# Performance work log

Measured on AMD Instinct MI355X. Metric: run time of the kernel, lower is better.

## Reference

```python
import jax, jax.numpy as jnp
import numpy as np


def setup_inputs() -> dict:
    key = jax.random.key(0)
    kq, kk, kv = jax.random.split(key, 3)
    B, H, S, D = 2, 16, 2048, 64
    Q = jax.random.normal(kq, (B, H, S, D), dtype=jnp.float32)
    K = jax.random.normal(kk, (B, H, S, D), dtype=jnp.float32)
    V = jax.random.normal(kv, (B, H, S, D), dtype=jnp.float32)
    # causal mask: 1 = keep, 0 = masked (masked_fill on mask == 0)
    mask = jnp.tril(jnp.ones((S, S), dtype=bool))[None, None, :, :]
    return {"V": V, "Q": Q, "K": K, "Fk": D, "mask": mask}


def reference(V, Q, K, Fk, mask):
    scale = 1.0 / jnp.sqrt(jnp.asarray(Fk, dtype=jnp.float32))
    # [B,H,S,S] scores
    C = jnp.einsum("bhqd,bhkd->bhqk", Q, K) * scale
    C = jnp.where(mask, C, jnp.asarray(-1e9, dtype=C.dtype))
    C = jax.nn.softmax(C, axis=-1)
    return jnp.einsum("bhqk,bhkd->bhqd", C, V)
```

## Files before the change

### kernel.cpp

```cpp
#include <hip/hip_runtime.h>
#include <hip/hip_bf16.h>

typedef __bf16 bf16x8 __attribute__((ext_vector_type(8)));
typedef __bf16 bf16x4 __attribute__((ext_vector_type(4)));
typedef __bf16 bf16x2 __attribute__((ext_vector_type(2)));
typedef float f32x4 __attribute__((ext_vector_type(4)));
typedef float f32x16 __attribute__((ext_vector_type(16)));

#define S_LEN 2048
#define D_DIM 64
#define NQT   32

static __device__ __forceinline__ unsigned pk2(float a, float b) {
  bf16x2 t; t[0] = (__bf16)a; t[1] = (__bf16)b;
  return __builtin_bit_cast(unsigned, t);
}

__global__ __launch_bounds__(256) void preprocess_kernel(
    const float* __restrict__ Kg, const float* __restrict__ Vg,
    unsigned char* __restrict__ Kb, unsigned char* __restrict__ Vt) {
  __shared__ float buf[2048];
  const int tid  = threadIdx.x;
  const int tile = blockIdx.x;
  const float* kg = Kg + (long)tile * 2048;
  const float* vg = Vg + (long)tile * 2048;
  unsigned char* kb = Kb + (long)tile * 4096;
  unsigned char* vt = Vt + (long)tile * 4096;

  const int l = tid & 63, f = tid >> 6, h = l >> 5;

  {
    const float* kr = kg + (l & 31) * 64 + f * 16 + h * 8;
    float4 a = *reinterpret_cast<const float4*>(kr);
    float4 b = *reinterpret_cast<const float4*>(kr + 4);
    bf16x8 t;
    t[0]=(__bf16)a.x; t[1]=(__bf16)a.y; t[2]=(__bf16)a.z; t[3]=(__bf16)a.w;
    t[4]=(__bf16)b.x; t[5]=(__bf16)b.y; t[6]=(__bf16)b.z; t[7]=(__bf16)b.w;
    *reinterpret_cast<bf16x8*>(kb + tid * 16) = t;
  }
  #pragma unroll
  for (int i = 0; i < 2; ++i) {
    int idx = tid + 256 * i;
    *reinterpret_cast<float4*>(buf + idx * 4) =
        *reinterpret_cast<const float4*>(vg + idx * 4);
  }
  __syncthreads();
  {
    int dt = f >> 1, ks = f & 1;
    int d  = dt * 32 + (l & 31);
    int k0 = ks * 16 + h * 8;
    bf16x8 t;
    #pragma unroll
    for (int j = 0; j < 8; ++j) t[j] = (__bf16)buf[(k0 + j) * 64 + d];
    *reinterpret_cast<bf16x8*>(vt + tid * 16) = t;
  }
}

__global__ __launch_bounds__(256, 2) void attn_fwd_q64(
    const float* __restrict__ Qg, const unsigned char* __restrict__ Kb,
    const unsigned char* __restrict__ Vt, float* __restrict__ Og) {
  __shared__ float o_sm[4][32][68];
  __shared__ float m_sm[4][32];
  __shared__ float l_sm[4][32];

  const int tid  = threadIdx.x;
  const int lane = tid & 63;
  const int w    = tid >> 6;
  const int qc   = lane & 31;
  const int h    = lane >> 5;

  const int b  = blockIdx.x;
  const int e  = b & 7;
  const int s  = b >> 3;
  const int bh = e + 8 * (s >> 4);
  const int pi = s & 15;
  const long base = (long)bh * (S_LEN * D_DIM);

  const unsigned char* kb_bh = Kb + (long)bh * 64 * 4096 + lane * 16;
  const unsigned char* vt_bh = Vt + (long)bh * 64 * 4096 + lane * 16;

  bf16x8 kfr[4], vfr[4];
  auto ldK = [&](int kt) {
    const unsigned char* p = kb_bh + (long)kt * 4096;
    #pragma unroll
    for (int t = 0; t < 4; ++t)
      kfr[t] = *reinterpret_cast<const bf16x8*>(p + t * 1024);
  };
  auto ldV = [&](int kt) {
    const unsigned char* p = vt_bh + (long)kt * 4096;
    #pragma unroll
    for (int t = 0; t < 4; ++t)
      vfr[t] = *reinterpret_cast<const bf16x8*>(p + t * 1024);
  };

  auto process = [&](f32x16& sa, float& m_run, float& l_run,
                     f32x16& po0, f32x16& po1) {
    float rmax;
    {
      float a0 = fmaxf(fmaxf(sa[0], sa[1]),  fmaxf(sa[2], sa[3]));
      float a1 = fmaxf(fmaxf(sa[4], sa[5]),  fmaxf(sa[6], sa[7]));
      float a2 = fmaxf(fmaxf(sa[8], sa[9]),  fmaxf(sa[10], sa[11]));
      float a3 = fmaxf(fmaxf(sa[12], sa[13]), fmaxf(sa[14], sa[15]));
      rmax = fmaxf(fmaxf(a0, a1), fmaxf(a2, a3));
      rmax = fmaxf(rmax, __shfl_xor(rmax, 32));
    }
    if (__any(rmax > m_run + 8.0f)) {
      float mn    = fmaxf(m_run, rmax);
      float alpha = exp2f(m_run - mn);
      m_run = mn;
      l_run *= alpha;
      #pragma unroll
      for (int r = 0; r < 16; ++r) {
        float ar = __shfl(alpha, (r & 3) + 8 * (r >> 2) + 4 * h);
        po0[r] *= ar;
        po1[r] *= ar;
      }
    }
    #pragma unroll
    for (int r = 0; r < 16; ++r) sa[r] = exp2f(sa[r] - m_run);
    {
      float s0 = (sa[0] + sa[1]) + (sa[2] + sa[3]);
      float s1 = (sa[4] + sa[5]) + (sa[6] + sa[7]);
      float s2 = (sa[8] + sa[9]) + (sa[10] + sa[11]);
      float s3 = (sa[12] + sa[13]) + (sa[14] + sa[15]);
      float rs = (s0 + s1) + (s2 + s3);
      l_run += rs + __shfl_xor(rs, 32);
    }
    bf16x8 pa0, pa1;
    {
      unsigned k0 = pk2(sa[0], sa[1]),   k1 = pk2(sa[2], sa[3]);
      unsigned k2 = pk2(sa[4], sa[5]),   k3 = pk2(sa[6], sa[7]);
      unsigned k4 = pk2(sa[8], sa[9]),   k5 = pk2(sa[10], sa[11]);
      unsigned k6 = pk2(sa[12], sa[13]), k7 = pk2(sa[14], sa[15]);
      unsigned x02 = h ? k0 : k2, x13 = h ? k1 : k3;
      unsigned x46 = h ? k4 : k6, x57 = h ? k5 : k7;
      unsigned p02 = (unsigned)__shfl_xor((int)x02, 32);
      unsigned p13 = (unsigned)__shfl_xor((int)x13, 32);
      unsigned p46 = (unsigned)__shfl_xor((int)x46, 32);
      unsigned p57 = (unsigned)__shfl_xor((int)x57, 32);
      union { unsigned u[4]; bf16x8 v; } a2, b2;
      a2.u[0] = h ? p02 : k0;  a2.u[1] = h ? p13 : k1;
      a2.u[2] = h ? k2 : p02;  a2.u[3] = h ? k3 : p13;
      b2.u[0] = h ? p46 : k4;  b2.u[1] = h ? p57 : k5;
      b2.u[2] = h ? k6 : p46;  b2.u[3] = h ? k7 : p57;
      pa0 = a2.v;
      pa1 = b2.v;
    }
    __builtin_amdgcn_s_setprio(1);
    po0 = __builtin_amdgcn_mfma_f32_32x32x16_bf16(pa0, vfr[0], po0, 0, 0, 0);
    po0 = __builtin_amdgcn_mfma_f32_32x32x16_bf16(pa1, vfr[1], po0, 0, 0, 0);
    po1 = __builtin_amdgcn_mfma_f32_32x32x16_bf16(pa0, vfr[2], po1, 0, 0, 0);
    po1 = __builtin_amdgcn_mfma_f32_32x32x16_bf16(pa1, vfr[3], po1, 0, 0, 0);
    __builtin_amdgcn_s_setprio(0);
  };

  auto submerge = [&](const f32x16& po0, const f32x16& po1,
                      float m_run, float l_run, int qbase) {
    #pragma unroll
    for (int r = 0; r < 16; ++r) {
      int crow = (r & 3) + 8 * (r >> 2) + 4 * h;
      o_sm[w][crow][qc]      = po0[r];
      o_sm[w][crow][qc + 32] = po1[r];
    }
    if (h == 0) { m_sm[w][qc] = m_run; l_sm[w][qc] = l_run; }
    __syncthreads();
    {
      const int q  = tid >> 3;
      const int d0 = (tid & 7) * 8;
      float m0 = m_sm[0][q], m1 = m_sm[1][q];
      float m2 = m_sm[2][q], m3 = m_sm[3][q];
      float M  = fmaxf(fmaxf(m0, m1), fmaxf(m2, m3));
      float a0 = exp2f(m0 - M), a1 = exp2f(m1 - M);
      float a2 = exp2f(m2 - M), a3 = exp2f(m3 - M);
      float inv = 1.0f / (a0 * l_sm[0][q] + a1 * l_sm[1][q]
                        + a2 * l_sm[2][q] + a3 * l_sm[3][q]);
      float* og = Og + base + (long)(qbase + q) * D_DIM + d0;
      #pragma unroll
      for (int half = 0; half < 2; ++half) {
        float4 x0 = *reinterpret_cast<const float4*>(&o_sm[0][q][d0 + 4 * half]);
        float4 x1 = *reinterpret_cast<const float4*>(&o_sm[1][q][d0 + 4 * half]);
        float4 x2 = *reinterpret_cast<const float4*>(&o_sm[2][q][d0 + 4 * half]);
        float4 x3 = *reinterpret_cast<const float4*>(&o_sm[3][q][d0 + 4 * half]);
        float4 o;
        o.x = (a0 * x0.x + a1 * x1.x + a2 * x2.x + a3 * x3.x) * inv;
        o.y = (a0 * x0.y + a1 * x1.y + a2 * x2.y + a3 * x3.y) * inv;
        o.z = (a0 * x0.z + a1 * x1.z + a2 * x2.z + a3 * x3.z) * inv;
        o.w = (a0 * x0.w + a1 * x1.w + a2 * x2.w + a3 * x3.w) * inv;
        *reinterpret_cast<float4*>(og + 4 * half) = o;
      }
    }
  };

  for (int phase = 0; phase < 2; ++phase) {
    const int g  = phase ? pi : (31 - pi);
    const int q0 = g * 64;
    const int NT = 2 * g + 2;

    bf16x8 qfA[4], qfB[4];
    {
      const float qsc = 0.125f * 1.44269504f;
      const float* qpA = Qg + base + (long)(q0 + qc) * D_DIM + h * 8;
      const float* qpB = qpA + 32 * D_DIM;
      #pragma unroll
      for (int t = 0; t < 4; ++t) {
        float4 f0 = *reinterpret_cast<const float4*>(qpA + t * 16);
        float4 f1 = *reinterpret_cast<const float4*>(qpA + t * 16 + 4);
        bf16x8 q;
        q[0]=(__bf16)(f0.x*qsc); q[1]=(__bf16)(f0.y*qsc);
        q[2]=(__bf16)(f0.z*qsc); q[3]=(__bf16)(f0.w*qsc);
        q[4]=(__bf16)(f1.x*qsc); q[5]=(__bf16)(f1.y*qsc);
        q[6]=(__bf16)(f1.z*qsc); q[7]=(__bf16)(f1.w*qsc);
        qfA[t] = q;
        f0 = *reinterpret_cast<const float4*>(qpB + t * 16);
        f1 = *reinterpret_cast<const float4*>(qpB + t * 16 + 4);
        q[0]=(__bf16)(f0.x*qsc); q[1]=(__bf16)(f0.y*qsc);
        q[2]=(__bf16)(f0.z*qsc); q[3]=(__bf16)(f0.w*qsc);
        q[4]=(__bf16)(f1.x*qsc); q[5]=(__bf16)(f1.y*qsc);
        q[6]=(__bf16)(f1.z*qsc); q[7]=(__bf16)(f1.w*qsc);
        qfB[t] = q;
      }
    }

    f32x16 poA0, poA1, poB0, poB1;
    #pragma unroll
    for (int r = 0; r < 16; ++r) { poA0[r]=0.f; poA1[r]=0.f; poB0[r]=0.f; poB1[r]=0.f; }
    float mA = -1e30f, lA = 0.f, mB = -1e30f, lB = 0.f;

    ldK(w);
    ldV(w);

    for (int kt = w; kt < NT; kt += 4) {
      const bool more = (kt + 4 < NT);
      const bool doA  = (kt != NT - 1);

      f32x16 saA, saB;
      __builtin_amdgcn_s_setprio(1);
      if (doA) {
        #pragma unroll
        for (int r = 0; r < 16; ++r) saA[r] = 0.f;
        #pragma unroll
        for (int t = 0; t < 4; ++t)
          saA = __builtin_amdgcn_mfma_f32_32x32x16_bf16(kfr[t], qfA[t], saA, 0, 0, 0);
      }
      #pragma unroll
      for (int r = 0; r < 16; ++r) saB[r] = 0.f;
      #pragma unroll
      for (int t = 0; t < 4; ++t)
        saB = __builtin_amdgcn_mfma_f32_32x32x16_bf16(kfr[t], qfB[t], saB, 0, 0, 0);
      __builtin_amdgcn_s_setprio(0);

      if (more) ldK(kt + 4);

      if (kt == NT - 2) {
        #pragma unroll
        for (int r = 0; r < 16; ++r)
          if (((r & 3) + 8 * (r >> 2) + 4 * h) > qc) saA[r] = -1e30f;
      }
      if (kt == NT - 1) {
        #pragma unroll
        for (int r = 0; r < 16; ++r)
          if (((r & 3) + 8 * (r >> 2) + 4 * h) > qc) saB[r] = -1e30f;
      }

      if (doA) process(saA, mA, lA, poA0, poA1);
      process(saB, mB, lB, poB0, poB1);

      if (more) ldV(kt + 4);
    }

    if (phase) __syncthreads();
    submerge(poA0, poA1, mA, lA, q0);
    __syncthreads();
    submerge(poB0, poB1, mB, lB, q0 + 32);
  }
}

__global__ __launch_bounds__(256) void attn_fwd_fallback(
    const float* __restrict__ Vg, const float* __restrict__ Qg,
    const float* __restrict__ Kg, float* __restrict__ Og) {
  __shared__ __align__(16) unsigned char k_lds[64 * 128];
  __shared__ __align__(16) unsigned char vt_lds[64 * 128];
  __shared__ __align__(16) unsigned char p_lds[4][16 * 128];

  const int tid  = threadIdx.x;
  const int lane = tid & 63;
  const int w    = tid >> 6;
  const int lr   = lane & 15;
  const int lg   = lane >> 4;
  const int swz  = (lr & 7) << 4;

  const int lb = blockIdx.x;
  const int e  = lb & 7;
  const int s  = lb >> 3;
  const int bh = e + 8 * (s >> 5);
  const int qs = s & 31;
  const int qt = (qs & 1) ? (NQT - 1 - (qs >> 1)) : (qs >> 1);
  const long base = (long)bh * (S_LEN * D_DIM);
  const int q0 = qt * 64;

  bf16x8 qf[2];
  {
    const float qsc = 0.125f * 1.44269504f;
    const float* qp = Qg + base + (q0 + w * 16 + lr) * D_DIM + lg * 8;
    #pragma unroll
    for (int c = 0; c < 2; ++c) {
      float4 f0 = *reinterpret_cast<const float4*>(qp + c * 32);
      float4 f1 = *reinterpret_cast<const float4*>(qp + c * 32 + 4);
      bf16x8 t;
      t[0]=(__bf16)(f0.x*qsc); t[1]=(__bf16)(f0.y*qsc);
      t[2]=(__bf16)(f0.z*qsc); t[3]=(__bf16)(f0.w*qsc);
      t[4]=(__bf16)(f1.x*qsc); t[5]=(__bf16)(f1.y*qsc);
      t[6]=(__bf16)(f1.z*qsc); t[7]=(__bf16)(f1.w*qsc);
      qf[c] = t;
    }
  }
  bf16x8 onesf;
  #pragma unroll
  for (int j = 0; j < 8; ++j) onesf[j] = (lr == 0) ? (__bf16)1.0f : (__bf16)0.0f;

  f32x4 po[4], pl;
  float m_run = -1e30f;
  #pragma unroll
  for (int j = 0; j < 4; ++j) po[j] = (f32x4){0.f,0.f,0.f,0.f};
  pl = (f32x4){0.f,0.f,0.f,0.f};

  float4 kreg[4];
  float  vreg[16];
  const int d_ = lane;
  const int kb = w;

  auto load_regs = [&](int kt) {
    const float* kg = Kg + base + kt * (64 * D_DIM);
    #pragma unroll
    for (int i = 0; i < 4; ++i) {
      int idx = tid + 256 * i;
      int r = idx >> 4, f4 = idx & 15;
      kreg[i] = *reinterpret_cast<const float4*>(kg + r * 64 + f4 * 4);
    }
    const float* vg = Vg + base + kt * (64 * D_DIM);
    #pragma unroll
    for (int j = 0; j < 8; ++j) {
      vreg[j]     = vg[(kb * 8 + j) * 64 + d_];
      vreg[8 + j] = vg[((kb + 4) * 8 + j) * 64 + d_];
    }
  };
  auto write_buf = [&]() {
    #pragma unroll
    for (int i = 0; i < 4; ++i) {
      int idx = tid + 256 * i;
      int r = idx >> 4, f4 = idx & 15;
      bf16x4 t;
      t[0]=(__bf16)kreg[i].x; t[1]=(__bf16)kreg[i].y;
      t[2]=(__bf16)kreg[i].z; t[3]=(__bf16)kreg[i].w;
      int b = r * 128 + ((f4 * 8) ^ ((r & 7) << 4));
      *reinterpret_cast<bf16x4*>(&k_lds[b]) = t;
    }
    bf16x8 t0, t1;
    #pragma unroll
    for (int j = 0; j < 8; ++j) { t0[j] = (__bf16)vreg[j]; t1[j] = (__bf16)vreg[8+j]; }
    int b0 = d_ * 128 + ((kb * 16) ^ ((d_ & 7) << 4));
    int b1 = d_ * 128 + (((kb + 4) * 16) ^ ((d_ & 7) << 4));
    *reinterpret_cast<bf16x8*>(&vt_lds[b0]) = t0;
    *reinterpret_cast<bf16x8*>(&vt_lds[b1]) = t1;
  };

  load_regs(0);
  write_buf();
  __syncthreads();

  for (int kt = 0; kt <= qt; ++kt) {
    const bool last = (kt == qt);
    if (!last) load_regs(kt + 1);

    f32x4 sa[4];
    #pragma unroll
    for (int ct = 0; ct < 4; ++ct) sa[ct] = (f32x4){0.f,0.f,0.f,0.f};
    #pragma unroll
    for (int ct = 0; ct < 4; ++ct) {
      #pragma unroll
      for (int c = 0; c < 2; ++c) {
        int b = (ct * 16 + lr) * 128 + ((lg * 16 + c * 64) ^ swz);
        bf16x8 kf = *reinterpret_cast<const bf16x8*>(&k_lds[b]);
        sa[ct] = __builtin_amdgcn_mfma_f32_16x16x32_bf16(kf, qf[c], sa[ct], 0, 0, 0);
      }
    }
    if (last) {
      #pragma unroll
      for (int ct = 0; ct < 4; ++ct)
        #pragma unroll
        for (int j = 0; j < 4; ++j)
          if (ct * 16 + lg * 4 + j > w * 16 + lr) sa[ct][j] = -1e30f;
    }
    float rmax = sa[0][0];
    #pragma unroll
    for (int ct = 0; ct < 4; ++ct)
      #pragma unroll
      for (int j = 0; j < 4; ++j) rmax = fmaxf(rmax, sa[ct][j]);
    rmax = fmaxf(rmax, __shfl_xor(rmax, 16));
    rmax = fmaxf(rmax, __shfl_xor(rmax, 32));
    float mn    = fmaxf(m_run, rmax);
    float alpha = exp2f(m_run - mn);
    m_run = mn;
    #pragma unroll
    for (int ct = 0; ct < 4; ++ct) {
      bf16x4 t;
      #pragma unroll
      for (int j = 0; j < 4; ++j) t[j] = (__bf16)exp2f(sa[ct][j] - mn);
      int b = lr * 128 + ((ct * 32 + lg * 8) ^ swz);
      *reinterpret_cast<bf16x4*>(&p_lds[w][b]) = t;
    }
    float aj[4];
    #pragma unroll
    for (int j = 0; j < 4; ++j) aj[j] = __shfl(alpha, (lane & 48) | (lg * 4 + j));
    #pragma unroll
    for (int j = 0; j < 4; ++j) {
      pl[j] *= aj[j];
      #pragma unroll
      for (int dt = 0; dt < 4; ++dt) po[dt][j] *= aj[j];
    }
    #pragma unroll
    for (int c = 0; c < 2; ++c) {
      int ab = lr * 128 + ((lg * 16 + c * 64) ^ swz);
      bf16x8 pa = *reinterpret_cast<const bf16x8*>(&p_lds[w][ab]);
      pl = __builtin_amdgcn_mfma_f32_16x16x32_bf16(pa, onesf, pl, 0, 0, 0);
      #pragma unroll
      for (int dt = 0; dt < 4; ++dt) {
        int vb_ = (dt * 16 + lr) * 128 + ((lg * 16 + c * 64) ^ swz);
        bf16x8 vb = *reinterpret_cast<const bf16x8*>(&vt_lds[vb_]);
        po[dt] = __builtin_amdgcn_mfma_f32_16x16x32_bf16(pa, vb, po[dt], 0, 0, 0);
      }
    }
    if (!last) {
      __syncthreads();
      write_buf();
      __syncthreads();
    }
  }
  #pragma unroll
  for (int j = 0; j < 4; ++j) {
    float lv  = __shfl(pl[j], lane & 48);
    float inv = 1.0f / lv;
    int row = q0 + w * 16 + lg * 4 + j;
    #pragma unroll
    for (int dt = 0; dt < 4; ++dt)
      Og[base + row * D_DIM + dt * 16 + lr] = po[dt][j] * inv;
  }
}

extern "C" void kernel_launch(void* const* d_in, const int* in_sizes, int n_in,
                              void* d_out, int out_size, void* d_ws, size_t ws_size,
                              hipStream_t stream) {
  const float* V = (const float*)d_in[0];
  const float* Q = (const float*)d_in[1];
  const float* K = (const float*)d_in[2];
  float* O = (float*)d_out;
  const size_t need = (size_t)2 * 32 * 64 * 4096;
  if (ws_size >= need) {
    unsigned char* Kb = (unsigned char*)d_ws;
    unsigned char* Vt = Kb + (size_t)32 * 64 * 4096;
    preprocess_kernel<<<dim3(2048), dim3(256), 0, stream>>>(K, V, Kb, Vt);
    attn_fwd_q64<<<dim3(512), dim3(256), 0, stream>>>(Q, Kb, Vt, O);
  } else {
    attn_fwd_fallback<<<dim3(1024), dim3(256), 0, stream>>>(V, Q, K, O);
  }
}
```

Before: 58.05 us.

## Split KV tiles across eight waves per block instead of four

Doubles the block size of the attention kernel to 512 threads so eight waves each take every eighth key tile, and widens the shared-memory merge to combine eight partial softmax states. The merge is rewritten so each thread produces one float4 of output. The aim is more parallelism per query block and better latency hiding on the per-block critical path. In exchange it doubles the LDS used for partial outputs, adds more merge work, and asks for four 512-thread blocks per CU in launch bounds, which tightens the register budget.

```diff
diff --git a/kernel.cpp b/kernel.cpp
--- a/kernel.cpp
+++ b/kernel.cpp
@@ -10,6 +10,7 @@
 #define S_LEN 2048
 #define D_DIM 64
 #define NQT   32
+#define NW    8
 
 static __device__ __forceinline__ unsigned pk2(float a, float b) {
   bf16x2 t; t[0] = (__bf16)a; t[1] = (__bf16)b;
@@ -56,12 +57,12 @@
   }
 }
 
-__global__ __launch_bounds__(256, 2) void attn_fwd_q64(
+__global__ __launch_bounds__(512, 4) void attn_fwd_q64(
     const float* __restrict__ Qg, const unsigned char* __restrict__ Kb,
     const unsigned char* __restrict__ Vt, float* __restrict__ Og) {
-  __shared__ float o_sm[4][32][68];
-  __shared__ float m_sm[4][32];
-  __shared__ float l_sm[4][32];
+  __shared__ float o_sm[NW][32][68];
+  __shared__ float m_sm[NW][32];
+  __shared__ float l_sm[NW][32];
 
   const int tid  = threadIdx.x;
   const int lane = tid & 63;
@@ -165,29 +166,25 @@
     if (h == 0) { m_sm[w][qc] = m_run; l_sm[w][qc] = l_run; }
     __syncthreads();
     {
-      const int q  = tid >> 3;
-      const int d0 = (tid & 7) * 8;
-      float m0 = m_sm[0][q], m1 = m_sm[1][q];
-      float m2 = m_sm[2][q], m3 = m_sm[3][q];
-      float M  = fmaxf(fmaxf(m0, m1), fmaxf(m2, m3));
-      float a0 = exp2f(m0 - M), a1 = exp2f(m1 - M);
-      float a2 = exp2f(m2 - M), a3 = exp2f(m3 - M);
-      float inv = 1.0f / (a0 * l_sm[0][q] + a1 * l_sm[1][q]
-                        + a2 * l_sm[2][q] + a3 * l_sm[3][q]);
-      float* og = Og + base + (long)(qbase + q) * D_DIM + d0;
-      #pragma unroll
-      for (int half = 0; half < 2; ++half) {
-        float4 x0 = *reinterpret_cast<const float4*>(&o_sm[0][q][d0 + 4 * half]);
-        float4 x1 = *reinterpret_cast<const float4*>(&o_sm[1][q][d0 + 4 * half]);
-        float4 x2 = *reinterpret_cast<const float4*>(&o_sm[2][q][d0 + 4 * half]);
-        float4 x3 = *reinterpret_cast<const float4*>(&o_sm[3][q][d0 + 4 * half]);
-        float4 o;
-        o.x = (a0 * x0.x + a1 * x1.x + a2 * x2.x + a3 * x3.x) * inv;
-        o.y = (a0 * x0.y + a1 * x1.y + a2 * x2.y + a3 * x3.y) * inv;
-        o.z = (a0 * x0.z + a1 * x1.z + a2 * x2.z + a3 * x3.z) * inv;
-        o.w = (a0 * x0.w + a1 * x1.w + a2 * x2.w + a3 * x3.w) * inv;
-        *reinterpret_cast<float4*>(og + 4 * half) = o;
-      }
+      const int q  = tid >> 4;
+      const int d0 = (tid & 15) * 4;
+      float M = -1e30f;
+      float mm[NW];
+      #pragma unroll
+      for (int i = 0; i < NW; ++i) { mm[i] = m_sm[i][q]; M = fmaxf(M, mm[i]); }
+      float lsum = 0.f, aa[NW];
+      #pragma unroll
+      for (int i = 0; i < NW; ++i) { aa[i] = exp2f(mm[i] - M); lsum += aa[i] * l_sm[i][q]; }
+      float inv = 1.0f / lsum;
+      float4 acc = make_float4(0.f, 0.f, 0.f, 0.f);
+      #pragma unroll
+      for (int i = 0; i < NW; ++i) {
+        float4 x = *reinterpret_cast<const float4*>(&o_sm[i][q][d0]);
+        acc.x += aa[i] * x.x; acc.y += aa[i] * x.y;
+        acc.z += aa[i] * x.z; acc.w += aa[i] * x.w;
+      }
+      acc.x *= inv; acc.y *= inv; acc.z *= inv; acc.w *= inv;
+      *reinterpret_cast<float4*>(Og + base + (long)(qbase + q) * D_DIM + d0) = acc;
     }
   };
 
@@ -229,8 +226,8 @@
     ldK(w);
     ldV(w);
 
-    for (int kt = w; kt < NT; kt += 4) {
-      const bool more = (kt + 4 < NT);
+    for (int kt = w; kt < NT; kt += NW) {
+      const bool more = (kt + NW < NT);
       const bool doA  = (kt != NT - 1);
 
       f32x16 saA, saB;
@@ -249,7 +246,7 @@
         saB = __builtin_amdgcn_mfma_f32_32x32x16_bf16(kfr[t], qfB[t], saB, 0, 0, 0);
       __builtin_amdgcn_s_setprio(0);
 
-      if (more) ldK(kt + 4);
+      if (more) ldK(kt + NW);
 
       if (kt == NT - 2) {
         #pragma unroll
@@ -265,7 +262,7 @@
       if (doA) process(saA, mA, lA, poA0, poA1);
       process(saB, mB, lB, poB0, poB1);
 
-      if (more) ldV(kt + 4);
+      if (more) ldV(kt + NW);
     }
 
     if (phase) __syncthreads();
@@ -459,7 +456,7 @@
     unsigned char* Kb = (unsigned char*)d_ws;
     unsigned char* Vt = Kb + (size_t)32 * 64 * 4096;
     preprocess_kernel<<<dim3(2048), dim3(256), 0, stream>>>(K, V, Kb, Vt);
-    attn_fwd_q64<<<dim3(512), dim3(256), 0, stream>>>(Q, Kb, Vt, O);
+    attn_fwd_q64<<<dim3(512), dim3(512), 0, stream>>>(Q, Kb, Vt, O);
   } else {
     attn_fwd_fallback<<<dim3(1024), dim3(256), 0, stream>>>(V, Q, K, O);
   }
```

Result: slower. 222.1 us (+282.7%).
